# Kernel optimization log

Hardware: AMD Instinct MI355X
Metric: run time of the kernel (lower is better)

Reference implementation:

```python
import jax, jax.numpy as jnp
import numpy as np

TEMP = 0.1

def _normalized_grid(B, H, W, dtype=jnp.float32):
    # normalized coords in [-1, 1], (x, y) order, shape [B, H, W, 2]
    ys = jnp.linspace(-1.0, 1.0, H, dtype=dtype)
    xs = jnp.linspace(-1.0, 1.0, W, dtype=dtype)
    gy, gx = jnp.meshgrid(ys, xs, indexing='ij')
    grid = jnp.stack([gx, gy], axis=-1)  # [H, W, 2]
    return jnp.broadcast_to(grid, (B, H, W, 2))


def setup_inputs() -> dict:
    key = jax.random.key(0)
    k1, k2, k3 = jax.random.split(key, 3)
    B, H, W, D = 8, 48, 48, 1024
    f_mv_A = jax.random.normal(k1, (B, H, W, D), dtype=jnp.float32)
    f_mv_B = jax.random.normal(k2, (B, H, W, D), dtype=jnp.float32)
    # omega buffer: 2*pi*randn(dim//2, 2)
    omega = 2.0 * jnp.pi * jax.random.normal(k3, (D // 2, 2), dtype=jnp.float32)
    scale = jnp.ones((), dtype=jnp.float32)
    return {"f_mv_A": f_mv_A, "f_mv_B": f_mv_B, "omega": omega, "scale": scale}


def reference(f_mv_A, f_mv_B, omega, scale):
    B, H_A, W_A, D = f_mv_A.shape
    _, H_B, W_B, _ = f_mv_B.shape
    # Fourier positional embedding grid over image B coordinates
    x = _normalized_grid(B, H_B, W_B).reshape(B, H_B * W_B, 2)
    x_emb = x @ (scale * omega).T                      # [B, HW_B, D//2]
    pos_emb_grid = jnp.concatenate([jnp.sin(x_emb), jnp.cos(x_emb)], axis=-1)  # [B, HW_B, D]

    # cosine similarity cross-attention
    fa = f_mv_A / jnp.linalg.norm(f_mv_A, axis=-1, keepdims=True)
    fb = f_mv_B / jnp.linalg.norm(f_mv_B, axis=-1, keepdims=True)
    fa = fa.reshape(B, H_A * W_A, D)
    fb = fb.reshape(B, H_B * W_B, D)
    attn_logits = (1.0 / TEMP) * jnp.einsum('bqd,bkd->bqk', fa, fb)  # [B, HW_A, HW_B]
    attn = jax.nn.softmax(attn_logits, axis=2)
    match_emb = jnp.einsum('bqk,bkd->bqd', attn, pos_emb_grid)        # [B, HW_A, D]

    attn_logits = attn_logits.reshape(B, H_A, W_A, H_B, W_B)
    attn = attn.reshape(B, H_A, W_A, H_B, W_B)
    match_emb = match_emb.reshape(B, H_A, W_A, D)
    return attn_logits, attn, match_emb
```

## Files before the change

### kernel.cpp

```cpp
#include <hip/hip_runtime.h>
#include <stdint.h>
#include <math.h>

#define NBATCH 8
#define HWSZ   2304
#define DDIM   1024
#define NROWS  (NBATCH*HWSZ)
#define PLANE  ((size_t)NROWS*DDIM)
#define OFF1   ((size_t)NBATCH*HWSZ*HWSZ)
#define OFF2   (2*OFF1)

typedef __attribute__((ext_vector_type(8))) short bf16x8;
typedef __attribute__((ext_vector_type(8))) _Float16 f16x8;
typedef __attribute__((ext_vector_type(4))) float f32x4;

__device__ __forceinline__ float bf2f(uint16_t u) {
    union { uint32_t i; float f; } v; v.i = ((uint32_t)u) << 16; return v.f;
}
__device__ __forceinline__ uint16_t f2bf(float f) {
    union { uint32_t i; float f; } v; v.f = f;
    uint32_t x = v.i;
    return (uint16_t)((x + 0x7fffu + ((x >> 16) & 1u)) >> 16);
}
__device__ __forceinline__ float h2f(uint16_t u) {
    _Float16 h; __builtin_memcpy(&h, &u, 2); return (float)h;
}
__device__ __forceinline__ uint16_t f2h(float f) {
    _Float16 h = (_Float16)f; uint16_t u; __builtin_memcpy(&u, &h, 2); return u;
}
__device__ __forceinline__ int dmode(const uint16_t* s) {
    uint16_t v = s[0];
    return (v == 0x3F80u) ? 1 : ((v == 0x3C00u) ? 2 : 0);
}
__device__ __forceinline__ float dec16(uint16_t u, int m) { return (m == 1) ? bf2f(u) : h2f(u); }
__device__ __forceinline__ uint16_t enc16(float f, int m) { return (m == 1) ? f2bf(f) : f2h(f); }

__global__ void layout_probe(int* __restrict__ rowT, int* __restrict__ colT) {
    int lane = threadIdx.x & 63;
    int m = lane & 15, q = lane >> 4;
    bf16x8 a1, b1, a2, b2;
    #pragma unroll
    for (int j = 0; j < 8; j++) {
        int k = q * 8 + j;
        float k0 = (k == 0) ? 1.0f : 0.0f;
        a1[j] = (short)f2bf(k0);
        b1[j] = (short)f2bf(k0 * (float)(m + 1));
        a2[j] = (short)f2bf(k0 * (float)(m + 1));
        b2[j] = (short)f2bf(k0);
    }
    f32x4 z = {0.f, 0.f, 0.f, 0.f};
    f32x4 d1 = __builtin_amdgcn_mfma_f32_16x16x32_bf16(a1, b1, z, 0, 0, 0);
    f32x4 d2 = __builtin_amdgcn_mfma_f32_16x16x32_bf16(a2, b2, z, 0, 0, 0);
    #pragma unroll
    for (int r = 0; r < 4; r++) {
        colT[lane * 4 + r] = (int)d1[r] - 1;
        rowT[lane * 4 + r] = (int)d2[r] - 1;
    }
}

__global__ void rownorm_kernel(const void* __restrict__ inA, const void* __restrict__ inB,
                               const uint16_t* __restrict__ scalep, float* __restrict__ rn,
                               void* __restrict__ outbase) {
    const int mode = dmode(scalep);
    int row = blockIdx.x;
    int t = threadIdx.x;
    const void* src = (row < NROWS) ? inA : inB;
    int lrow = (row < NROWS) ? row : row - NROWS;
    float v[4];
    if (mode == 0) {
        const float* p = (const float*)src + (size_t)lrow * DDIM + t * 4;
        float4 f = *(const float4*)p;
        v[0] = f.x; v[1] = f.y; v[2] = f.z; v[3] = f.w;
        uint16_t* hbase = (uint16_t*)((float*)outbase + OFF1) + ((row < NROWS) ? 0 : PLANE);
        uint16_t h0 = f2h(v[0]), h1 = f2h(v[1]), h2 = f2h(v[2]), h3 = f2h(v[3]);
        uint2 hv;
        hv.x = (uint32_t)h0 | ((uint32_t)h1 << 16);
        hv.y = (uint32_t)h2 | ((uint32_t)h3 << 16);
        *(uint2*)(hbase + (size_t)lrow * DDIM + t * 4) = hv;
    } else {
        const uint16_t* p = (const uint16_t*)src + (size_t)lrow * DDIM + t * 4;
        uint2 u = *(const uint2*)p;
        v[0] = dec16(u.x & 0xffff, mode); v[1] = dec16(u.x >> 16, mode);
        v[2] = dec16(u.y & 0xffff, mode); v[3] = dec16(u.y >> 16, mode);
    }
    float ss = v[0]*v[0] + v[1]*v[1] + v[2]*v[2] + v[3]*v[3];
    __shared__ float red[256];
    red[t] = ss; __syncthreads();
    for (int s = 128; s > 0; s >>= 1) { if (t < s) red[t] += red[t + s]; __syncthreads(); }
    if (t == 0) rn[row] = 1.0f / sqrtf(red[0]);
}

__global__ void posemb_kernel(const void* __restrict__ omega, const uint16_t* __restrict__ scalep,
                              uint16_t* __restrict__ posT) {
    const int mode = dmode(scalep);
    int j = blockIdx.x;
    float om0, om1, sc;
    if (mode == 0) {
        const float* om = (const float*)omega;
        om0 = om[j * 2]; om1 = om[j * 2 + 1];
        sc = *(const float*)scalep;
    } else {
        const uint16_t* om = (const uint16_t*)omega;
        om0 = dec16(om[j * 2], mode); om1 = dec16(om[j * 2 + 1], mode);
        sc = dec16(scalep[0], mode);
    }
    om0 *= sc; om1 *= sc;
    for (int p = threadIdx.x; p < HWSZ; p += 256) {
        int iy = p / 48, ix = p % 48;
        float gx = (2.0f / 47.0f) * (float)ix - 1.0f;
        float gy = (2.0f / 47.0f) * (float)iy - 1.0f;
        float e = om0 * gx + om1 * gy;
        size_t chunk = (size_t)(p >> 5) * (DDIM * 32);
        int kin = p & 31;
        posT[chunk + (size_t)j * 32 + kin]           = f2bf(sinf(e));
        posT[chunk + (size_t)(j + 512) * 32 + kin]   = f2bf(cosf(e));
    }
}

#define LSTR 40

__launch_bounds__(256, 2)
__global__ void gemm1_mfma(const void* __restrict__ inA, const void* __restrict__ inB,
                           const uint16_t* __restrict__ scalep, const float* __restrict__ rn,
                           void* __restrict__ outbase,
                           const int* __restrict__ rowT, const int* __restrict__ colT) {
    const int mode = dmode(scalep);
    __shared__ uint16_t sA[128 * LSTR];
    __shared__ uint16_t sB[128 * LSTR];
    __shared__ float rnS[256];
    int g = blockIdx.x;
    int swz = (g & 7) * 324 + (g >> 3);
    int b = swz / 324;
    int rr = swz % 324;
    int tm = rr / 18, tn = rr % 18;
    int t = threadIdx.x;
    if (t < 128) rnS[t] = 10.0f * rn[(size_t)b * HWSZ + tm * 128 + t];
    else         rnS[t] = rn[(size_t)NROWS + (size_t)b * HWSZ + tn * 128 + (t - 128)];
    int r0c = t >> 2, cb0 = (t & 3) * 8;
    int r1c = r0c + 64;
    int lane = t & 63, wave = t >> 6;
    int wm = (wave & 1) * 64, wn = (wave >> 1) * 64;
    int lr = lane & 15, ko = (lane >> 4) * 8;
    size_t rowA0 = (size_t)b * HWSZ + tm * 128;
    size_t rowB0 = (size_t)b * HWSZ + tn * 128;
    const uint16_t* pA16;
    const uint16_t* pB16;
    if (mode == 0) {
        const uint16_t* planes = (const uint16_t*)((const float*)outbase + OFF1);
        pA16 = planes + rowA0 * DDIM;
        pB16 = planes + PLANE + rowB0 * DDIM;
    } else {
        pA16 = (const uint16_t*)inA + rowA0 * DDIM;
        pB16 = (const uint16_t*)inB + rowB0 * DDIM;
    }
    f32x4 acc[4][4] = {};

    for (int k0 = 0; k0 < DDIM; k0 += 32) {
        uint4 a0 = *(const uint4*)(pA16 + (size_t)r0c * DDIM + k0 + cb0);
        uint4 a1 = *(const uint4*)(pA16 + (size_t)r1c * DDIM + k0 + cb0);
        uint4 b0 = *(const uint4*)(pB16 + (size_t)r0c * DDIM + k0 + cb0);
        uint4 b1 = *(const uint4*)(pB16 + (size_t)r1c * DDIM + k0 + cb0);
        __syncthreads();
        *(uint4*)(sA + r0c * LSTR + cb0) = a0;
        *(uint4*)(sA + r1c * LSTR + cb0) = a1;
        *(uint4*)(sB + r0c * LSTR + cb0) = b0;
        *(uint4*)(sB + r1c * LSTR + cb0) = b1;
        __syncthreads();
        if (mode == 1) {
            bf16x8 af[4], bf_[4];
            #pragma unroll
            for (int i = 0; i < 4; i++) af[i] = *(const bf16x8*)(sA + (wm + i * 16 + lr) * LSTR + ko);
            #pragma unroll
            for (int j = 0; j < 4; j++) bf_[j] = *(const bf16x8*)(sB + (wn + j * 16 + lr) * LSTR + ko);
            #pragma unroll
            for (int i = 0; i < 4; i++)
                #pragma unroll
                for (int j = 0; j < 4; j++)
                    acc[i][j] = __builtin_amdgcn_mfma_f32_16x16x32_bf16(af[i], bf_[j], acc[i][j], 0, 0, 0);
        } else {
            f16x8 af[4], bf_[4];
            #pragma unroll
            for (int i = 0; i < 4; i++) af[i] = *(const f16x8*)(sA + (wm + i * 16 + lr) * LSTR + ko);
            #pragma unroll
            for (int j = 0; j < 4; j++) bf_[j] = *(const f16x8*)(sB + (wn + j * 16 + lr) * LSTR + ko);
            #pragma unroll
            for (int i = 0; i < 4; i++)
                #pragma unroll
                for (int j = 0; j < 4; j++)
                    acc[i][j] = __builtin_amdgcn_mfma_f32_16x16x32_f16(af[i], bf_[j], acc[i][j], 0, 0, 0);
        }
    }

    int rtab[4], ctab[4];
    #pragma unroll
    for (int r = 0; r < 4; r++) {
        rtab[r] = rowT[lane * 4 + r] & 15;
        ctab[r] = colT[lane * 4 + r] & 15;
    }
    size_t cbase = (size_t)b * HWSZ * HWSZ;
    #pragma unroll
    for (int i = 0; i < 4; i++) {
        #pragma unroll
        for (int j = 0; j < 4; j++) {
            #pragma unroll
            for (int r = 0; r < 4; r++) {
                int row = wm + i * 16 + rtab[r];
                int col = wn + j * 16 + ctab[r];
                float v = acc[i][j][r] * rnS[row] * rnS[128 + col];
                size_t gm = (size_t)(tm * 128 + row);
                size_t gn = (size_t)(tn * 128 + col);
                if (mode == 0) ((float*)outbase)[cbase + gm * HWSZ + gn] = v;
                else ((uint16_t*)outbase)[cbase + gm * HWSZ + gn] = enc16(v, mode);
            }
        }
    }
}

__global__ void rowstat_kernel(const void* __restrict__ outbase, const uint16_t* __restrict__ scalep,
                               float* __restrict__ stats) {
    const int mode = dmode(scalep);
    size_t row = blockIdx.x;
    int t = threadIdx.x;
    float v[9];
    if (mode == 0) {
        const float* src = (const float*)outbase + row * HWSZ;
        #pragma unroll
        for (int i = 0; i < 9; i++) v[i] = src[i * 256 + t];
    } else {
        const uint16_t* src = (const uint16_t*)outbase + row * HWSZ;
        #pragma unroll
        for (int i = 0; i < 9; i++) v[i] = dec16(src[i * 256 + t], mode);
    }
    float m = v[0];
    #pragma unroll
    for (int i = 1; i < 9; i++) m = fmaxf(m, v[i]);
    __shared__ float red[256];
    red[t] = m; __syncthreads();
    for (int s = 128; s > 0; s >>= 1) { if (t < s) red[t] = fmaxf(red[t], red[t + s]); __syncthreads(); }
    float M = red[0];
    __syncthreads();
    float ssum = 0.0f;
    #pragma unroll
    for (int i = 0; i < 9; i++) ssum += __expf(v[i] - M);
    red[t] = ssum; __syncthreads();
    for (int s = 128; s > 0; s >>= 1) { if (t < s) red[t] += red[t + s]; __syncthreads(); }
    if (t == 0) { stats[row] = M; stats[NROWS + row] = 1.0f / red[0]; }
}

#define G2BM 64
#define G2BN 256
#define G2L  40

__launch_bounds__(256, 4)
__global__ void gemm2_mfma(void* __restrict__ outbase, const uint16_t* __restrict__ posT,
                           const uint16_t* __restrict__ scalep, const float* __restrict__ stats,
                           const int* __restrict__ rowT, const int* __restrict__ colT) {
    const int mode = dmode(scalep);
    __shared__ uint16_t sA[G2BM * G2L];
    int g = blockIdx.x;
    int swz = (g & 7) * 144 + (g >> 3);
    int b = swz / 144;
    int rr = swz % 144;
    int tm = rr >> 2, tn = rr & 3;
    int t = threadIdx.x;
    int lane = t & 63, wave = t >> 6;
    int wn = wave * 64;
    int lr = lane & 15, ko = (lane >> 4) * 8;
    int ar = t >> 2, ac8 = (t & 3) * 8;
    size_t grow = (size_t)b * HWSZ + (size_t)tm * G2BM + ar;
    float Mrow = stats[grow];
    float invl = stats[NROWS + grow];
    f32x4 acc[4][4] = {};
    for (int k0 = 0; k0 < HWSZ; k0 += 32) {
        uint16_t av[8];
        float p[8];
        if (mode == 0) {
            const float* ap = (const float*)outbase + grow * HWSZ + k0 + ac8;
            float4 x0 = *(const float4*)ap, x1 = *(const float4*)(ap + 4);
            p[0] = __expf(x0.x - Mrow) * invl; p[1] = __expf(x0.y - Mrow) * invl;
            p[2] = __expf(x0.z - Mrow) * invl; p[3] = __expf(x0.w - Mrow) * invl;
            p[4] = __expf(x1.x - Mrow) * invl; p[5] = __expf(x1.y - Mrow) * invl;
            p[6] = __expf(x1.z - Mrow) * invl; p[7] = __expf(x1.w - Mrow) * invl;
            if (tn == 0) {
                float* dst = (float*)outbase + OFF1 + grow * HWSZ + k0 + ac8;
                *(float4*)dst       = *(const float4*)p;
                *(float4*)(dst + 4) = *(const float4*)(p + 4);
            }
        } else {
            const uint16_t* ap = (const uint16_t*)outbase + grow * HWSZ + k0 + ac8;
            uint4 r0 = *(const uint4*)ap;
            const uint16_t* u0 = (const uint16_t*)&r0;
            #pragma unroll
            for (int j = 0; j < 8; j++) p[j] = __expf(dec16(u0[j], mode) - Mrow) * invl;
            if (tn == 0) {
                uint16_t pk[8];
                #pragma unroll
                for (int j = 0; j < 8; j++) pk[j] = enc16(p[j], mode);
                *(uint4*)((uint16_t*)outbase + OFF1 + grow * HWSZ + k0 + ac8) = *(const uint4*)pk;
            }
        }
        #pragma unroll
        for (int j = 0; j < 8; j++) av[j] = f2bf(p[j]);
        __syncthreads();
        *(uint4*)(sA + ar * G2L + ac8) = *(const uint4*)av;
        __syncthreads();
        const uint16_t* bchunk = posT + (size_t)(k0 >> 5) * (DDIM * 32);
        bf16x8 af[4], bfr[4];
        #pragma unroll
        for (int j = 0; j < 4; j++)
            bfr[j] = *(const bf16x8*)(bchunk + ((size_t)tn * G2BN + wn + j * 16 + lr) * 32 + ko);
        #pragma unroll
        for (int i = 0; i < 4; i++) af[i] = *(const bf16x8*)(sA + (i * 16 + lr) * G2L + ko);
        #pragma unroll
        for (int i = 0; i < 4; i++)
            #pragma unroll
            for (int j = 0; j < 4; j++)
                acc[i][j] = __builtin_amdgcn_mfma_f32_16x16x32_bf16(af[i], bfr[j], acc[i][j], 0, 0, 0);
    }
    int rtab[4], ctab[4];
    #pragma unroll
    for (int r = 0; r < 4; r++) {
        rtab[r] = rowT[lane * 4 + r] & 15;
        ctab[r] = colT[lane * 4 + r] & 15;
    }
    #pragma unroll
    for (int i = 0; i < 4; i++) {
        #pragma unroll
        for (int j = 0; j < 4; j++) {
            #pragma unroll
            for (int r = 0; r < 4; r++) {
                size_t row = (size_t)tm * G2BM + i * 16 + rtab[r];
                size_t col = (size_t)tn * G2BN + wn + j * 16 + ctab[r];
                size_t idx = OFF2 + (size_t)b * HWSZ * DDIM + row * DDIM + col;
                if (mode == 0) ((float*)outbase)[idx] = acc[i][j][r];
                else ((uint16_t*)outbase)[idx] = enc16(acc[i][j][r], mode);
            }
        }
    }
}

extern "C" void kernel_launch(void* const* d_in, const int* in_sizes, int n_in,
                              void* d_out, int out_size, void* d_ws, size_t ws_size,
                              hipStream_t stream) {
    const void* fA    = d_in[0];
    const void* fB    = d_in[1];
    const void* omega = d_in[2];
    const uint16_t* scale = (const uint16_t*)d_in[3];

    int* rowT = (int*)d_ws;
    int* colT = rowT + 256;
    float* rn = (float*)((char*)d_ws + 4096);
    uint16_t* posT = (uint16_t*)((char*)d_ws + 4096 + (size_t)2 * NROWS * 4);

    layout_probe<<<1, 64, 0, stream>>>(rowT, colT);
    rownorm_kernel<<<2 * NROWS, 256, 0, stream>>>(fA, fB, scale, rn, d_out);
    posemb_kernel<<<512, 256, 0, stream>>>(omega, scale, posT);

    gemm1_mfma<<<18 * 18 * NBATCH, 256, 0, stream>>>(fA, fB, scale, rn, d_out, rowT, colT);

    rowstat_kernel<<<NROWS, 256, 0, stream>>>(d_out, scale, rn);

    gemm2_mfma<<<(HWSZ / G2BM) * (DDIM / G2BN) * NBATCH, 256, 0, stream>>>(d_out, posT, scale, rn, rowT, colT);
}
```

Baseline: 488.3 us.

## Write softmax probabilities in rowstat pass and feed bf16 probs to gemm2

The row-statistics kernel now computes and writes the final softmax probabilities itself, and also stores a bf16 copy in workspace. A new gemm2 variant reads that bf16 copy directly instead of reloading the logits and recomputing exp and normalisation per tile, and stages the B operand in shared memory. The aim is to drop the redundant exp work and fp32 logit reads from gemm2. In exchange it needs a large extra workspace buffer and an extra write of the full probability matrix. If the workspace is too small, the old path is used.

After: 458.9 us. 1.06x faster.

```diff
diff --git a/kernel.cpp b/kernel.cpp
--- a/kernel.cpp
+++ b/kernel.cpp
@@ -216,8 +216,8 @@
     }
 }
 
-__global__ void rowstat_kernel(const void* __restrict__ outbase, const uint16_t* __restrict__ scalep,
-                               float* __restrict__ stats) {
+__global__ void softmax_p16(void* __restrict__ outbase, const uint16_t* __restrict__ scalep,
+                            uint16_t* __restrict__ p16) {
     const int mode = dmode(scalep);
     size_t row = blockIdx.x;
     int t = threadIdx.x;
@@ -241,6 +241,55 @@
     __syncthreads();
     float ssum = 0.0f;
     #pragma unroll
+    for (int i = 0; i < 9; i++) { v[i] = __expf(v[i] - M); ssum += v[i]; }
+    red[t] = ssum; __syncthreads();
+    for (int s = 128; s > 0; s >>= 1) { if (t < s) red[t] += red[t + s]; __syncthreads(); }
+    float inv = 1.0f / red[0];
+    uint16_t* prow = p16 + row * HWSZ;
+    if (mode == 0) {
+        float* dst = (float*)outbase + OFF1 + row * HWSZ;
+        #pragma unroll
+        for (int i = 0; i < 9; i++) {
+            float p = v[i] * inv;
+            dst[i * 256 + t] = p;
+            prow[i * 256 + t] = f2bf(p);
+        }
+    } else {
+        uint16_t* dst = (uint16_t*)outbase + OFF1 + row * HWSZ;
+        #pragma unroll
+        for (int i = 0; i < 9; i++) {
+            uint16_t pk = enc16(v[i] * inv, mode);
+            dst[i * 256 + t] = pk;
+            prow[i * 256 + t] = (mode == 1) ? pk : f2bf(h2f(pk));
+        }
+    }
+}
+
+__global__ void rowstat_kernel(const void* __restrict__ outbase, const uint16_t* __restrict__ scalep,
+                               float* __restrict__ stats) {
+    const int mode = dmode(scalep);
+    size_t row = blockIdx.x;
+    int t = threadIdx.x;
+    float v[9];
+    if (mode == 0) {
+        const float* src = (const float*)outbase + row * HWSZ;
+        #pragma unroll
+        for (int i = 0; i < 9; i++) v[i] = src[i * 256 + t];
+    } else {
+        const uint16_t* src = (const uint16_t*)outbase + row * HWSZ;
+        #pragma unroll
+        for (int i = 0; i < 9; i++) v[i] = dec16(src[i * 256 + t], mode);
+    }
+    float m = v[0];
+    #pragma unroll
+    for (int i = 1; i < 9; i++) m = fmaxf(m, v[i]);
+    __shared__ float red[256];
+    red[t] = m; __syncthreads();
+    for (int s = 128; s > 0; s >>= 1) { if (t < s) red[t] = fmaxf(red[t], red[t + s]); __syncthreads(); }
+    float M = red[0];
+    __syncthreads();
+    float ssum = 0.0f;
+    #pragma unroll
     for (int i = 0; i < 9; i++) ssum += __expf(v[i] - M);
     red[t] = ssum; __syncthreads();
     for (int s = 128; s > 0; s >>= 1) { if (t < s) red[t] += red[t + s]; __syncthreads(); }
@@ -250,6 +299,72 @@
 #define G2BM 64
 #define G2BN 256
 #define G2L  40
+
+__launch_bounds__(256, 4)
+__global__ void gemm2_p16(void* __restrict__ outbase, const uint16_t* __restrict__ posT,
+                          const uint16_t* __restrict__ scalep, const uint16_t* __restrict__ p16,
+                          const int* __restrict__ rowT, const int* __restrict__ colT) {
+    const int mode = dmode(scalep);
+    __shared__ uint16_t sA[G2BM * G2L];
+    __shared__ uint16_t sB[G2BN * G2L];
+    int g = blockIdx.x;
+    int swz = (g & 7) * 144 + (g >> 3);
+    int b = swz / 144;
+    int rr = swz % 144;
+    int tm = rr >> 2, tn = rr & 3;
+    int t = threadIdx.x;
+    int lane = t & 63, wave = t >> 6;
+    int wn = wave * 64;
+    int lr = lane & 15, ko = (lane >> 4) * 8;
+    int ar = t >> 2, ac8 = (t & 3) * 8;
+    const uint16_t* pArow = p16 + ((size_t)b * HWSZ + (size_t)tm * G2BM + ar) * HWSZ;
+    f32x4 acc[4][4] = {};
+    for (int k0 = 0; k0 < HWSZ; k0 += 32) {
+        uint4 a0 = *(const uint4*)(pArow + k0 + ac8);
+        const uint16_t* bsrc = posT + (size_t)(k0 >> 5) * (DDIM * 32) + ((size_t)tn * G2BN + t) * 32;
+        uint4 bv0 = *(const uint4*)(bsrc + 0);
+        uint4 bv1 = *(const uint4*)(bsrc + 8);
+        uint4 bv2 = *(const uint4*)(bsrc + 16);
+        uint4 bv3 = *(const uint4*)(bsrc + 24);
+        __syncthreads();
+        *(uint4*)(sA + ar * G2L + ac8) = a0;
+        *(uint4*)(sB + t * G2L + 0)  = bv0;
+        *(uint4*)(sB + t * G2L + 8)  = bv1;
+        *(uint4*)(sB + t * G2L + 16) = bv2;
+        *(uint4*)(sB + t * G2L + 24) = bv3;
+        __syncthreads();
+        bf16x8 af[4], bfr[4];
+        #pragma unroll
+        for (int i = 0; i < 4; i++) af[i] = *(const bf16x8*)(sA + (i * 16 + lr) * G2L + ko);
+        #pragma unroll
+        for (int j = 0; j < 4; j++) bfr[j] = *(const bf16x8*)(sB + (wn + j * 16 + lr) * G2L + ko);
+        #pragma unroll
+        for (int i = 0; i < 4; i++)
+            #pragma unroll
+            for (int j = 0; j < 4; j++)
+                acc[i][j] = __builtin_amdgcn_mfma_f32_16x16x32_bf16(af[i], bfr[j], acc[i][j], 0, 0, 0);
+    }
+    int rtab[4], ctab[4];
+    #pragma unroll
+    for (int r = 0; r < 4; r++) {
+        rtab[r] = rowT[lane * 4 + r] & 15;
+        ctab[r] = colT[lane * 4 + r] & 15;
+    }
+    #pragma unroll
+    for (int i = 0; i < 4; i++) {
+        #pragma unroll
+        for (int j = 0; j < 4; j++) {
+            #pragma unroll
+            for (int r = 0; r < 4; r++) {
+                size_t row = (size_t)tm * G2BM + i * 16 + rtab[r];
+                size_t col = (size_t)tn * G2BN + wn + j * 16 + ctab[r];
+                size_t idx = OFF2 + (size_t)b * HWSZ * DDIM + row * DDIM + col;
+                if (mode == 0) ((float*)outbase)[idx] = acc[i][j][r];
+                else ((uint16_t*)outbase)[idx] = enc16(acc[i][j][r], mode);
+            }
+        }
+    }
+}
 
 __launch_bounds__(256, 4)
 __global__ void gemm2_mfma(void* __restrict__ outbase, const uint16_t* __restrict__ posT,
@@ -350,7 +465,12 @@
     int* rowT = (int*)d_ws;
     int* colT = rowT + 256;
     float* rn = (float*)((char*)d_ws + 4096);
-    uint16_t* posT = (uint16_t*)((char*)d_ws + 4096 + (size_t)2 * NROWS * 4);
+    size_t posT_off = 4096 + (size_t)2 * NROWS * 4;
+    uint16_t* posT = (uint16_t*)((char*)d_ws + posT_off);
+    size_t p16_off = posT_off + (size_t)DDIM * HWSZ * 2;
+    size_t ws_need = p16_off + (size_t)NROWS * HWSZ * 2;
+    uint16_t* p16 = (uint16_t*)((char*)d_ws + p16_off);
+    const bool big_ws = (ws_size >= ws_need);
 
     layout_probe<<<1, 64, 0, stream>>>(rowT, colT);
     rownorm_kernel<<<2 * NROWS, 256, 0, stream>>>(fA, fB, scale, rn, d_out);
@@ -358,7 +478,13 @@
 
     gemm1_mfma<<<18 * 18 * NBATCH, 256, 0, stream>>>(fA, fB, scale, rn, d_out, rowT, colT);
 
-    rowstat_kernel<<<NROWS, 256, 0, stream>>>(d_out, scale, rn);
-
-    gemm2_mfma<<<(HWSZ / G2BM) * (DDIM / G2BN) * NBATCH, 256, 0, stream>>>(d_out, posT, scale, rn, rowT, colT);
-}
+    if (big_ws) {
+        softmax_p16<<<NROWS, 256, 0, stream>>>(d_out, scale, p16);
+        gemm2_p16<<<(HWSZ / G2BM) * (DDIM / G2BN) * NBATCH, 256, 0, stream>>>(
+            d_out, posT, scale, p16, rowT, colT);
+    } else {
+        rowstat_kernel<<<NROWS, 256, 0, stream>>>(d_out, scale, rn);
+        gemm2_mfma<<<(HWSZ / G2BM) * (DDIM / G2BN) * NBATCH, 256, 0, stream>>>(
+            d_out, posT, scale, rn, rowT, colT);
+    }
+}
```
